# Performance work log

Hardware: AMD Instinct MI355X
Metric: run time of the kernel (lower is better)

The kernel has to match this reference:

```python
import jax, jax.numpy as jnp
import numpy as np

EMB = 1024
HEADS = 16
HEAD_DIM = EMB // HEADS
SEQ = 2048
BATCH = 2
FF = 4 * EMB


def gelu_tanh(x):
    # matches the hand-rolled GELU: 0.5*x*(1+tanh(sqrt(2/pi)*(x+0.044715*x^3)))
    c = jnp.sqrt(jnp.asarray(2.0 / jnp.pi, dtype=x.dtype))
    return 0.5 * x * (1.0 + jnp.tanh(c * (x + 0.044715 * x ** 3)))


def layernorm(x, scale, shift, eps=1e-5):
    mean = jnp.mean(x, axis=-1, keepdims=True)
    var = jnp.var(x, axis=-1, keepdims=True)  # unbiased=False
    return scale * (x - mean) * jax.lax.rsqrt(var + eps) + shift


def setup_inputs() -> dict:
    key = jax.random.key(0)
    ks = jax.random.split(key, 10)
    s = 1.0 / np.sqrt(EMB)
    sf = 1.0 / np.sqrt(FF)
    return {
        "x": jax.random.normal(ks[0], (BATCH, SEQ, EMB), jnp.float32),
        "Wq": jax.random.uniform(ks[1], (EMB, EMB), jnp.float32, -s, s),
        "Wk": jax.random.uniform(ks[2], (EMB, EMB), jnp.float32, -s, s),
        "Wv": jax.random.uniform(ks[3], (EMB, EMB), jnp.float32, -s, s),
        "Wo": jax.random.uniform(ks[4], (EMB, EMB), jnp.float32, -s, s),
        "bo": jnp.zeros((EMB,), jnp.float32),
        "ln1_g": jnp.ones((EMB,), jnp.float32),
        "ln1_b": jnp.zeros((EMB,), jnp.float32),
        "ln2_g": jnp.ones((EMB,), jnp.float32),
        "ln2_b": jnp.zeros((EMB,), jnp.float32),
        "W1": jax.random.uniform(ks[5], (EMB, FF), jnp.float32, -s, s),
        "b1": jnp.zeros((FF,), jnp.float32),
        "W2": jax.random.uniform(ks[6], (FF, EMB), jnp.float32, -sf, sf),
        "b2": jnp.zeros((EMB,), jnp.float32),
    }


def reference(x, Wq, Wk, Wv, Wo, bo, ln1_g, ln1_b, ln2_g, ln2_b, W1, b1, W2, b2):
    b, n, d = x.shape
    shortcut = x
    h = layernorm(x, ln1_g, ln1_b)
    # projections -> [b, heads, n, head_dim]
    def split_heads(t):
        return t.reshape(b, n, HEADS, HEAD_DIM).transpose(0, 2, 1, 3)
    q = split_heads(h @ Wq)
    k = split_heads(h @ Wk)
    v = split_heads(h @ Wv)
    scores = jnp.einsum("bhqd,bhkd->bhqk", q, k)
    causal = jnp.triu(jnp.ones((n, n), dtype=bool), k=1)
    scores = jnp.where(causal, -jnp.inf, scores)
    weights = jax.nn.softmax(scores / jnp.sqrt(jnp.asarray(HEAD_DIM, x.dtype)), axis=-1)
    ctx = jnp.einsum("bhqk,bhkd->bhqd", weights, v)
    ctx = ctx.transpose(0, 2, 1, 3).reshape(b, n, d)
    attn_out = ctx @ Wo + bo
    x = attn_out + shortcut
    shortcut = x
    h = layernorm(x, ln2_g, ln2_b)
    ff = gelu_tanh(h @ W1 + b1) @ W2 + b2
    return ff + shortcut
```

## Files before the change

kernel.cpp:

```cpp
#include <hip/hip_runtime.h>

typedef __bf16 bf16x8 __attribute__((ext_vector_type(8)));
typedef float f32x4 __attribute__((ext_vector_type(4)));
typedef float f32x16 __attribute__((ext_vector_type(16)));
typedef unsigned int u32x4 __attribute__((ext_vector_type(4)));
typedef unsigned short u16;

#define EMB 1024
#define SEQ 2048
#define BATCH 2
#define HEADS 16
#define HEAD_DIM 64
#define FF 4096
#define ROWS (BATCH * SEQ)

#define QSCALE 0.18033688011112042f

static __device__ __forceinline__ u16 f2bf(float f) {
    unsigned int u = __builtin_bit_cast(unsigned int, f);
    unsigned int r = (u + 0x7FFFu + ((u >> 16) & 1u)) >> 16;
    return (u16)r;
}

static __device__ __forceinline__ unsigned int pack_bf_trunc(float a, float b) {
    return __builtin_amdgcn_perm(__builtin_bit_cast(unsigned int, a),
                                 __builtin_bit_cast(unsigned int, b), 0x07060302u);
}

static __device__ __forceinline__ void gload16(const u16* g, u16* l) {
    __builtin_amdgcn_global_load_lds(
        (const __attribute__((address_space(1))) unsigned int*)(const void*)g,
        (__attribute__((address_space(3))) unsigned int*)(void*)l, 16, 0, 0);
}

__global__ __launch_bounds__(256) void transpose_f32_to_bf16(
    const float* __restrict__ in, u16* __restrict__ out, int R, int C) {
    __shared__ float tile[32][33];
    int c0 = blockIdx.x * 32, r0 = blockIdx.y * 32;
    int tx = threadIdx.x & 31, ty = threadIdx.x >> 5;
#pragma unroll
    for (int i = 0; i < 32; i += 8)
        tile[ty + i][tx] = in[(size_t)(r0 + ty + i) * C + c0 + tx];
    __syncthreads();
#pragma unroll
    for (int i = 0; i < 32; i += 8)
        out[(size_t)(c0 + ty + i) * R + r0 + tx] = f2bf(tile[tx][ty + i]);
}

__global__ __launch_bounds__(256) void transpose4_f32_to_bf16(
    const float* __restrict__ s0, const float* __restrict__ s1,
    const float* __restrict__ s2, const float* __restrict__ s3,
    u16* __restrict__ d0, u16* __restrict__ d1,
    u16* __restrict__ d2, u16* __restrict__ d3) {
    __shared__ float tile[32][33];
    const float* in;
    u16* out;
    switch (blockIdx.z) {
        case 0: in = s0; out = d0; break;
        case 1: in = s1; out = d1; break;
        case 2: in = s2; out = d2; break;
        default: in = s3; out = d3; break;
    }
    int c0 = blockIdx.x * 32, r0 = blockIdx.y * 32;
    int tx = threadIdx.x & 31, ty = threadIdx.x >> 5;
#pragma unroll
    for (int i = 0; i < 32; i += 8)
        tile[ty + i][tx] = in[(size_t)(r0 + ty + i) * EMB + c0 + tx];
    __syncthreads();
#pragma unroll
    for (int i = 0; i < 32; i += 8)
        out[(size_t)(c0 + ty + i) * EMB + r0 + tx] = f2bf(tile[tx][ty + i]);
}

__global__ __launch_bounds__(256) void ln_kernel(
    const float* __restrict__ x, const float* __restrict__ gamma,
    const float* __restrict__ beta, u16* __restrict__ out) {
    int row = blockIdx.x;
    int t = threadIdx.x;
    float4 v = reinterpret_cast<const float4*>(x + (size_t)row * EMB)[t];
    float s = v.x + v.y + v.z + v.w;
    float s2 = v.x * v.x + v.y * v.y + v.z * v.z + v.w * v.w;
#pragma unroll
    for (int off = 1; off < 64; off <<= 1) {
        s += __shfl_xor(s, off);
        s2 += __shfl_xor(s2, off);
    }
    __shared__ float sm[8];
    int wid = t >> 6;
    if ((t & 63) == 0) { sm[wid] = s; sm[wid + 4] = s2; }
    __syncthreads();
    s = sm[0] + sm[1] + sm[2] + sm[3];
    s2 = sm[4] + sm[5] + sm[6] + sm[7];
    float mean = s * (1.0f / EMB);
    float var = s2 * (1.0f / EMB) - mean * mean;
    float inv = rsqrtf(var + 1e-5f);
    float4 gv = reinterpret_cast<const float4*>(gamma)[t];
    float4 bv = reinterpret_cast<const float4*>(beta)[t];
    ushort4 o;
    o.x = f2bf((v.x - mean) * inv * gv.x + bv.x);
    o.y = f2bf((v.y - mean) * inv * gv.y + bv.y);
    o.z = f2bf((v.z - mean) * inv * gv.z + bv.z);
    o.w = f2bf((v.w - mean) * inv * gv.w + bv.w);
    reinterpret_cast<ushort4*>(out + (size_t)row * EMB)[t] = o;
}

template <int EPI, int BN>
__global__ __launch_bounds__(256) void gemm_bf16(
    const u16* __restrict__ A, const u16* __restrict__ B, void* __restrict__ Cout,
    const float* __restrict__ bias, const float* __restrict__ resid,
    void* __restrict__ Cout2, void* __restrict__ Cout3,
    int M, int N, int K) {
    __shared__ u16 As[128 * 64];
    __shared__ u16 Bs[BN * 64];
    constexpr int MI = (BN == 128) ? 4 : 2;
    constexpr int BSW = BN / 32;
    int tm = blockIdx.x * 128;
    int tn = blockIdx.y * BN;
    int t = threadIdx.x;
    int lane = t & 63, wid = t >> 6;
    int wr, wc;
    if constexpr (BN == 128) { wr = (wid >> 1) * 64; wc = (wid & 1) * 64; }
    else { wr = wid * 32; wc = 0; }
    int l15 = lane & 15, g = lane >> 4;
    const u16* Abase = A + (size_t)tm * K;
    const u16* Bbase = B + (size_t)tn * K;
    f32x4 acc[MI][4] = {};
    for (int k0 = 0; k0 < K; k0 += 64) {
        __syncthreads();
#pragma unroll
        for (int p = 0; p < 4; ++p) {
            int chunk = (wid * 4 + p) * 64 + lane;
            int row = chunk >> 3, c8 = (chunk & 7) * 8;
            gload16(Abase + (size_t)row * K + k0 + c8, &As[(wid * 4 + p) * 512]);
        }
#pragma unroll
        for (int p = 0; p < BSW; ++p) {
            int chunk = (wid * BSW + p) * 64 + lane;
            int row = chunk >> 3, c8 = (chunk & 7) * 8;
            gload16(Bbase + (size_t)row * K + k0 + c8, &Bs[(wid * BSW + p) * 512]);
        }
        __syncthreads();
#pragma unroll
        for (int kc = 0; kc < 2; ++kc) {
            int ko = kc * 32 + g * 8;
            bf16x8 af[MI], bfr[4];
#pragma unroll
            for (int i = 0; i < MI; ++i)
                af[i] = *reinterpret_cast<const bf16x8*>(&As[(wr + i * 16 + l15) * 64 + ko]);
#pragma unroll
            for (int j = 0; j < 4; ++j)
                bfr[j] = *reinterpret_cast<const bf16x8*>(&Bs[(wc + j * 16 + l15) * 64 + ko]);
#pragma unroll
            for (int i = 0; i < MI; ++i)
#pragma unroll
                for (int j = 0; j < 4; ++j)
                    acc[i][j] = __builtin_amdgcn_mfma_f32_16x16x32_bf16(af[i], bfr[j], acc[i][j], 0, 0, 0);
        }
    }
    int mb = tm + wr + g * 4;
    int nb = tn + wc + l15;
#pragma unroll
    for (int i = 0; i < MI; ++i) {
#pragma unroll
        for (int j = 0; j < 4; ++j) {
            int n = nb + j * 16;
#pragma unroll
            for (int r = 0; r < 4; ++r) {
                int m = mb + i * 16 + r;
                float val = acc[i][j][r];
                if constexpr (EPI == 0) {
                    ((u16*)Cout)[(size_t)m * N + n] = f2bf(val);
                } else if constexpr (EPI == 1) {
                    ((float*)Cout)[(size_t)m * N + n] =
                        val + bias[n] + resid[(size_t)m * N + n];
                } else if constexpr (EPI == 2) {
                    float xg = val + bias[n];
                    float x3 = xg + 0.044715f * xg * xg * xg;
                    float tz = 0.7978845608028654f * x3;
                    float th = 1.0f - 2.0f / (1.0f + __expf(2.0f * tz));
                    ((u16*)Cout)[(size_t)m * N + n] = f2bf(0.5f * xg * (1.0f + th));
                } else {
                    if (n < 1024) {
                        ((u16*)Cout)[(size_t)m * 1024 + n] = f2bf(val * QSCALE);
                    } else if (n < 2048) {
                        ((u16*)Cout2)[(size_t)m * 1024 + (n - 1024)] = f2bf(val);
                    } else {
                        int bb = m >> 11, ss = m & 2047;
                        ((u16*)Cout3)[((size_t)(bb * EMB + (n - 2048))) * SEQ + ss] = f2bf(val);
                    }
                }
            }
        }
    }
}

__global__ __launch_bounds__(64, 2) void attn_kernel(
    const u16* __restrict__ Qb, const u16* __restrict__ Kb,
    const u16* __restrict__ Vt, u16* __restrict__ ctx) {
    int bh = blockIdx.x;
    int b = bh >> 4, h = bh & 15;
    int qc = 63 - (int)blockIdx.y;
    int lane = threadIdx.x;
    int l31 = lane & 31, hi = lane >> 5;
    int hi8 = hi * 8, hi4 = hi * 4;
    int qbase = qc * 32;

    const u16* Qrow = Qb + (size_t)(b * SEQ) * EMB + h * 64;
    const u16* Krow = Kb + (size_t)(b * SEQ) * EMB + h * 64;
    const u16* Vrow = Vt + (size_t)(b * EMB + h * 64) * SEQ;

    bf16x8 qf[4];
#pragma unroll
    for (int kc = 0; kc < 4; ++kc)
        qf[kc] = *reinterpret_cast<const bf16x8*>(
            Qrow + (size_t)(qbase + l31) * EMB + kc * 16 + hi8);

    f32x16 ctx_acc[2] = {};
    float mrun = -1e30f;
    float lrun = 0.f;
    int nkt = qc / 2 + 1;

    bf16x8 kcur[8];
#pragma unroll
    for (int i = 0; i < 8; ++i) {
        int kb = i >> 2, kc = i & 3;
        kcur[i] = *reinterpret_cast<const bf16x8*>(
            Krow + (size_t)(kb * 32 + l31) * EMB + kc * 16 + hi8);
    }

    for (int kt = 0; kt < nkt; ++kt) {
        int k0 = kt * 64;
        bool last = (kt == nkt - 1);
        bf16x8 vf[8];
#pragma unroll
        for (int i = 0; i < 8; ++i) {
            int ks = i >> 1, dt = i & 1;
            vf[i] = *reinterpret_cast<const bf16x8*>(
                Vrow + (size_t)(dt * 32 + l31) * SEQ + k0 + ks * 16 + hi8);
        }
        f32x16 sacc[2] = {};
#pragma unroll
        for (int kb = 0; kb < 2; ++kb)
#pragma unroll
            for (int kc = 0; kc < 4; ++kc)
                sacc[kb] = __builtin_amdgcn_mfma_f32_32x32x16_bf16(
                    kcur[kb * 4 + kc], qf[kc], sacc[kb], 0, 0, 0);
        if (kt + 1 < nkt) {
#pragma unroll
            for (int i = 0; i < 8; ++i) {
                int kb = i >> 2, kc = i & 3;
                kcur[i] = *reinterpret_cast<const bf16x8*>(
                    Krow + (size_t)(k0 + 64 + kb * 32 + l31) * EMB + kc * 16 + hi8);
            }
        }
        float sv[32];
        float tmax = -1e30f;
        if (last) {
            int q = qbase + l31;
#pragma unroll
            for (int kb = 0; kb < 2; ++kb)
#pragma unroll
                for (int r = 0; r < 16; ++r) {
                    int key = k0 + kb * 32 + (r & 3) + 8 * (r >> 2) + hi4;
                    float sx = (key > q) ? -1e30f : sacc[kb][r];
                    sv[kb * 16 + r] = sx;
                    tmax = fmaxf(tmax, sx);
                }
        } else {
#pragma unroll
            for (int kb = 0; kb < 2; ++kb)
#pragma unroll
                for (int r = 0; r < 16; ++r) {
                    float sx = sacc[kb][r];
                    sv[kb * 16 + r] = sx;
                    tmax = fmaxf(tmax, sx);
                }
        }
        tmax = fmaxf(tmax, __shfl_xor(tmax, 32));
        if (!__all(tmax <= mrun + 8.0f)) {
            float mnew = fmaxf(mrun, tmax);
            float corr = __builtin_amdgcn_exp2f(mrun - mnew);
            mrun = mnew;
            lrun *= corr;
            float corr_r[16];
#pragma unroll
            for (int r = 0; r < 16; ++r)
                corr_r[r] = __shfl(corr, (r & 3) + 8 * (r >> 2) + hi4);
#pragma unroll
            for (int dt = 0; dt < 2; ++dt)
#pragma unroll
                for (int r = 0; r < 16; ++r) ctx_acc[dt][r] *= corr_r[r];
        }
        float m = mrun;
        float psum = 0.f;
#pragma unroll
        for (int i = 0; i < 32; ++i) {
            float p = __builtin_amdgcn_exp2f(sv[i] - m);
            sv[i] = p;
            psum += p;
        }
        lrun += psum;
        bf16x8 pa[4];
#pragma unroll
        for (int ks = 0; ks < 4; ++ks) {
            int bse = (ks >> 1) * 16 + (ks & 1) * 8;
            unsigned int w0 = pack_bf_trunc(sv[bse + 1], sv[bse + 0]);
            unsigned int wA = pack_bf_trunc(sv[bse + 5], sv[bse + 4]);
            unsigned int w1 = pack_bf_trunc(sv[bse + 3], sv[bse + 2]);
            unsigned int wB = pack_bf_trunc(sv[bse + 7], sv[bse + 6]);
            asm("v_permlane32_swap_b32 %0, %1" : "+v"(w0), "+v"(wA));
            asm("v_permlane32_swap_b32 %0, %1" : "+v"(w1), "+v"(wB));
            u32x4 words = {w0, w1, wA, wB};
            pa[ks] = __builtin_bit_cast(bf16x8, words);
        }
#pragma unroll
        for (int ks = 0; ks < 4; ++ks)
#pragma unroll
            for (int dt = 0; dt < 2; ++dt)
                ctx_acc[dt] = __builtin_amdgcn_mfma_f32_32x32x16_bf16(
                    pa[ks], vf[ks * 2 + dt], ctx_acc[dt], 0, 0, 0);
    }
    lrun += __shfl_xor(lrun, 32);
    float linv = 1.0f / lrun;
    float li[16];
#pragma unroll
    for (int r = 0; r < 16; ++r)
        li[r] = __shfl(linv, (r & 3) + 8 * (r >> 2) + hi4);
#pragma unroll
    for (int dt = 0; dt < 2; ++dt)
#pragma unroll
        for (int r = 0; r < 16; ++r) {
            int q = qbase + (r & 3) + 8 * (r >> 2) + hi4;
            int d = h * 64 + dt * 32 + l31;
            ctx[(size_t)(b * SEQ + q) * EMB + d] = f2bf(ctx_acc[dt][r] * li[r]);
        }
}

extern "C" void kernel_launch(void* const* d_in, const int* in_sizes, int n_in,
                              void* d_out, int out_size, void* d_ws, size_t ws_size,
                              hipStream_t stream) {
    const float* x    = (const float*)d_in[0];
    const float* Wq   = (const float*)d_in[1];
    const float* Wk   = (const float*)d_in[2];
    const float* Wv   = (const float*)d_in[3];
    const float* Wo   = (const float*)d_in[4];
    const float* bo   = (const float*)d_in[5];
    const float* ln1g = (const float*)d_in[6];
    const float* ln1b = (const float*)d_in[7];
    const float* ln2g = (const float*)d_in[8];
    const float* ln2b = (const float*)d_in[9];
    const float* W1   = (const float*)d_in[10];
    const float* b1   = (const float*)d_in[11];
    const float* W2   = (const float*)d_in[12];
    const float* b2   = (const float*)d_in[13];

    char* ws = (char*)d_ws;
    size_t off = 0;
    auto alloc = [&](size_t bytes) {
        void* p = ws + off;
        off += (bytes + 255) & ~(size_t)255;
        return p;
    };
    u16* h1     = (u16*)alloc((size_t)ROWS * EMB * 2);
    u16* Wqkvt  = (u16*)alloc((size_t)3 * EMB * EMB * 2);
    u16* Wot    = (u16*)alloc((size_t)EMB * EMB * 2);
    u16* W1t    = (u16*)alloc((size_t)FF * EMB * 2);
    u16* W2t    = (u16*)alloc((size_t)EMB * FF * 2);
    u16* Qb     = (u16*)alloc((size_t)ROWS * EMB * 2);
    u16* Kb     = (u16*)alloc((size_t)ROWS * EMB * 2);
    u16* Vtb    = (u16*)alloc((size_t)BATCH * EMB * SEQ * 2);
    u16* ctxb   = (u16*)alloc((size_t)ROWS * EMB * 2);
    float* x2   = (float*)alloc((size_t)ROWS * EMB * 4);
    u16* h2     = (u16*)alloc((size_t)ROWS * EMB * 2);
    u16* ff1    = (u16*)alloc((size_t)ROWS * FF * 2);

    u16* Wqt = Wqkvt;
    u16* Wkt = Wqkvt + (size_t)EMB * EMB;
    u16* Wvt = Wqkvt + (size_t)2 * EMB * EMB;

    transpose4_f32_to_bf16<<<dim3(32, 32, 4), 256, 0, stream>>>(
        Wq, Wk, Wv, Wo, Wqt, Wkt, Wvt, Wot);
    transpose_f32_to_bf16<<<dim3(128, 32), 256, 0, stream>>>(W1, W1t, EMB, FF);
    transpose_f32_to_bf16<<<dim3(32, 128), 256, 0, stream>>>(W2, W2t, FF, EMB);

    ln_kernel<<<ROWS, 256, 0, stream>>>(x, ln1g, ln1b, h1);

    gemm_bf16<4, 128><<<dim3(32, 24), 256, 0, stream>>>(h1, Wqkvt, Qb, nullptr, nullptr,
                                                        Kb, Vtb, ROWS, 3072, EMB);

    attn_kernel<<<dim3(32, 64), 64, 0, stream>>>(Qb, Kb, Vtb, ctxb);

    gemm_bf16<1, 64><<<dim3(32, 16), 256, 0, stream>>>(ctxb, Wot, x2, bo, x,
                                                       nullptr, nullptr, ROWS, EMB, EMB);

    ln_kernel<<<ROWS, 256, 0, stream>>>(x2, ln2g, ln2b, h2);

    gemm_bf16<2, 128><<<dim3(32, 32), 256, 0, stream>>>(h2, W1t, ff1, b1, nullptr,
                                                        nullptr, nullptr, ROWS, FF, EMB);
    gemm_bf16<1, 64><<<dim3(32, 16), 256, 0, stream>>>(ff1, W2t, (float*)d_out, b2, x2,
                                                       nullptr, nullptr, ROWS, EMB, FF);
}
```

Before: 412.9 us.

## Use 64x64 GEMM tiles for N=1024 projections and 32-key attention tiles

Adds a BM template parameter so the Wo and W2 projection GEMMs run with 64x64 tiles, doubling the block count to fill more compute units. The attention kernel now iterates over 32-key tiles instead of 64, cutting wasted work on the causal diagonal tile and lowering register use. In exchange, the smaller GEMM tiles reduce operand reuse, and attention runs more loop iterations with more per-iteration softmax overhead.

New measurement: 414.9 us. About the same (+0.5%).

```diff
diff --git a/kernel.cpp b/kernel.cpp
--- a/kernel.cpp
+++ b/kernel.cpp
@@ -104,34 +104,37 @@
     reinterpret_cast<ushort4*>(out + (size_t)row * EMB)[t] = o;
 }
 
-template <int EPI, int BN>
+template <int EPI, int BM, int BN>
 __global__ __launch_bounds__(256) void gemm_bf16(
     const u16* __restrict__ A, const u16* __restrict__ B, void* __restrict__ Cout,
     const float* __restrict__ bias, const float* __restrict__ resid,
     void* __restrict__ Cout2, void* __restrict__ Cout3,
     int M, int N, int K) {
-    __shared__ u16 As[128 * 64];
+    __shared__ u16 As[BM * 64];
     __shared__ u16 Bs[BN * 64];
-    constexpr int MI = (BN == 128) ? 4 : 2;
+    constexpr int MI = (BM == 128 && BN == 128) ? 4 : 2;
+    constexpr int NJ = (BN == 128) ? 4 : ((BM == 128) ? 4 : 2);
+    constexpr int ASW = BM / 32;
     constexpr int BSW = BN / 32;
-    int tm = blockIdx.x * 128;
+    int tm = blockIdx.x * BM;
     int tn = blockIdx.y * BN;
     int t = threadIdx.x;
     int lane = t & 63, wid = t >> 6;
     int wr, wc;
-    if constexpr (BN == 128) { wr = (wid >> 1) * 64; wc = (wid & 1) * 64; }
-    else { wr = wid * 32; wc = 0; }
+    if constexpr (BM == 128 && BN == 128) { wr = (wid >> 1) * 64; wc = (wid & 1) * 64; }
+    else if constexpr (BM == 128) { wr = wid * 32; wc = 0; }
+    else { wr = (wid >> 1) * 32; wc = (wid & 1) * 32; }
     int l15 = lane & 15, g = lane >> 4;
     const u16* Abase = A + (size_t)tm * K;
     const u16* Bbase = B + (size_t)tn * K;
-    f32x4 acc[MI][4] = {};
+    f32x4 acc[MI][NJ] = {};
     for (int k0 = 0; k0 < K; k0 += 64) {
         __syncthreads();
 #pragma unroll
-        for (int p = 0; p < 4; ++p) {
-            int chunk = (wid * 4 + p) * 64 + lane;
+        for (int p = 0; p < ASW; ++p) {
+            int chunk = (wid * ASW + p) * 64 + lane;
             int row = chunk >> 3, c8 = (chunk & 7) * 8;
-            gload16(Abase + (size_t)row * K + k0 + c8, &As[(wid * 4 + p) * 512]);
+            gload16(Abase + (size_t)row * K + k0 + c8, &As[(wid * ASW + p) * 512]);
         }
 #pragma unroll
         for (int p = 0; p < BSW; ++p) {
@@ -143,17 +146,17 @@
 #pragma unroll
         for (int kc = 0; kc < 2; ++kc) {
             int ko = kc * 32 + g * 8;
-            bf16x8 af[MI], bfr[4];
+            bf16x8 af[MI], bfr[NJ];
 #pragma unroll
             for (int i = 0; i < MI; ++i)
                 af[i] = *reinterpret_cast<const bf16x8*>(&As[(wr + i * 16 + l15) * 64 + ko]);
 #pragma unroll
-            for (int j = 0; j < 4; ++j)
+            for (int j = 0; j < NJ; ++j)
                 bfr[j] = *reinterpret_cast<const bf16x8*>(&Bs[(wc + j * 16 + l15) * 64 + ko]);
 #pragma unroll
             for (int i = 0; i < MI; ++i)
 #pragma unroll
-                for (int j = 0; j < 4; ++j)
+                for (int j = 0; j < NJ; ++j)
                     acc[i][j] = __builtin_amdgcn_mfma_f32_16x16x32_bf16(af[i], bfr[j], acc[i][j], 0, 0, 0);
         }
     }
@@ -162,7 +165,7 @@
 #pragma unroll
     for (int i = 0; i < MI; ++i) {
 #pragma unroll
-        for (int j = 0; j < 4; ++j) {
+        for (int j = 0; j < NJ; ++j) {
             int n = nb + j * 16;
 #pragma unroll
             for (int r = 0; r < 4; ++r) {
@@ -218,63 +221,52 @@
     f32x16 ctx_acc[2] = {};
     float mrun = -1e30f;
     float lrun = 0.f;
-    int nkt = qc / 2 + 1;
-
-    bf16x8 kcur[8];
-#pragma unroll
-    for (int i = 0; i < 8; ++i) {
-        int kb = i >> 2, kc = i & 3;
-        kcur[i] = *reinterpret_cast<const bf16x8*>(
-            Krow + (size_t)(kb * 32 + l31) * EMB + kc * 16 + hi8);
-    }
+    int nkt = qc + 1;
+
+    bf16x8 kcur[4];
+#pragma unroll
+    for (int kc = 0; kc < 4; ++kc)
+        kcur[kc] = *reinterpret_cast<const bf16x8*>(
+            Krow + (size_t)l31 * EMB + kc * 16 + hi8);
 
     for (int kt = 0; kt < nkt; ++kt) {
-        int k0 = kt * 64;
+        int k0 = kt * 32;
         bool last = (kt == nkt - 1);
-        bf16x8 vf[8];
-#pragma unroll
-        for (int i = 0; i < 8; ++i) {
+        bf16x8 vf[4];
+#pragma unroll
+        for (int i = 0; i < 4; ++i) {
             int ks = i >> 1, dt = i & 1;
             vf[i] = *reinterpret_cast<const bf16x8*>(
                 Vrow + (size_t)(dt * 32 + l31) * SEQ + k0 + ks * 16 + hi8);
         }
-        f32x16 sacc[2] = {};
-#pragma unroll
-        for (int kb = 0; kb < 2; ++kb)
+        f32x16 sacc = {};
+#pragma unroll
+        for (int kc = 0; kc < 4; ++kc)
+            sacc = __builtin_amdgcn_mfma_f32_32x32x16_bf16(kcur[kc], qf[kc], sacc, 0, 0, 0);
+        if (kt + 1 < nkt) {
 #pragma unroll
             for (int kc = 0; kc < 4; ++kc)
-                sacc[kb] = __builtin_amdgcn_mfma_f32_32x32x16_bf16(
-                    kcur[kb * 4 + kc], qf[kc], sacc[kb], 0, 0, 0);
-        if (kt + 1 < nkt) {
-#pragma unroll
-            for (int i = 0; i < 8; ++i) {
-                int kb = i >> 2, kc = i & 3;
-                kcur[i] = *reinterpret_cast<const bf16x8*>(
-                    Krow + (size_t)(k0 + 64 + kb * 32 + l31) * EMB + kc * 16 + hi8);
-            }
-        }
-        float sv[32];
+                kcur[kc] = *reinterpret_cast<const bf16x8*>(
+                    Krow + (size_t)(k0 + 32 + l31) * EMB + kc * 16 + hi8);
+        }
+        float sv[16];
         float tmax = -1e30f;
         if (last) {
             int q = qbase + l31;
 #pragma unroll
-            for (int kb = 0; kb < 2; ++kb)
-#pragma unroll
-                for (int r = 0; r < 16; ++r) {
-                    int key = k0 + kb * 32 + (r & 3) + 8 * (r >> 2) + hi4;
-                    float sx = (key > q) ? -1e30f : sacc[kb][r];
-                    sv[kb * 16 + r] = sx;
-                    tmax = fmaxf(tmax, sx);
-                }
+            for (int r = 0; r < 16; ++r) {
+                int key = k0 + (r & 3) + 8 * (r >> 2) + hi4;
+                float sx = (key > q) ? -1e30f : sacc[r];
+                sv[r] = sx;
+                tmax = fmaxf(tmax, sx);
+            }
         } else {
 #pragma unroll
-            for (int kb = 0; kb < 2; ++kb)
-#pragma unroll
-                for (int r = 0; r < 16; ++r) {
-                    float sx = sacc[kb][r];
-                    sv[kb * 16 + r] = sx;
-                    tmax = fmaxf(tmax, sx);
-                }
+            for (int r = 0; r < 16; ++r) {
+                float sx = sacc[r];
+                sv[r] = sx;
+                tmax = fmaxf(tmax, sx);
+            }
         }
         tmax = fmaxf(tmax, __shfl_xor(tmax, 32));
         if (!__all(tmax <= mrun + 8.0f)) {
@@ -294,16 +286,16 @@
         float m = mrun;
         float psum = 0.f;
 #pragma unroll
-        for (int i = 0; i < 32; ++i) {
+        for (int i = 0; i < 16; ++i) {
             float p = __builtin_amdgcn_exp2f(sv[i] - m);
             sv[i] = p;
             psum += p;
         }
         lrun += psum;
-        bf16x8 pa[4];
-#pragma unroll
-        for (int ks = 0; ks < 4; ++ks) {
-            int bse = (ks >> 1) * 16 + (ks & 1) * 8;
+        bf16x8 pa[2];
+#pragma unroll
+        for (int ks = 0; ks < 2; ++ks) {
+            int bse = ks * 8;
             unsigned int w0 = pack_bf_trunc(sv[bse + 1], sv[bse + 0]);
             unsigned int wA = pack_bf_trunc(sv[bse + 5], sv[bse + 4]);
             unsigned int w1 = pack_bf_trunc(sv[bse + 3], sv[bse + 2]);
@@ -314,7 +306,7 @@
             pa[ks] = __builtin_bit_cast(bf16x8, words);
         }
 #pragma unroll
-        for (int ks = 0; ks < 4; ++ks)
+        for (int ks = 0; ks < 2; ++ks)
 #pragma unroll
             for (int dt = 0; dt < 2; ++dt)
                 ctx_acc[dt] = __builtin_amdgcn_mfma_f32_32x32x16_bf16(
@@ -385,18 +377,18 @@
 
     ln_kernel<<<ROWS, 256, 0, stream>>>(x, ln1g, ln1b, h1);
 
-    gemm_bf16<4, 128><<<dim3(32, 24), 256, 0, stream>>>(h1, Wqkvt, Qb, nullptr, nullptr,
-                                                        Kb, Vtb, ROWS, 3072, EMB);
+    gemm_bf16<4, 128, 128><<<dim3(32, 24), 256, 0, stream>>>(h1, Wqkvt, Qb, nullptr, nullptr,
+                                                             Kb, Vtb, ROWS, 3072, EMB);
 
     attn_kernel<<<dim3(32, 64), 64, 0, stream>>>(Qb, Kb, Vtb, ctxb);
 
-    gemm_bf16<1, 64><<<dim3(32, 16), 256, 0, stream>>>(ctxb, Wot, x2, bo, x,
-                                                       nullptr, nullptr, ROWS, EMB, EMB);
+    gemm_bf16<1, 64, 64><<<dim3(64, 16), 256, 0, stream>>>(ctxb, Wot, x2, bo, x,
+                                                           nullptr, nullptr, ROWS, EMB, EMB);
 
     ln_kernel<<<ROWS, 256, 0, stream>>>(x2, ln2g, ln2b, h2);
 
-    gemm_bf16<2, 128><<<dim3(32, 32), 256, 0, stream>>>(h2, W1t, ff1, b1, nullptr,
-                                                        nullptr, nullptr, ROWS, FF, EMB);
-    gemm_bf16<1, 64><<<dim3(32, 16), 256, 0, stream>>>(ff1, W2t, (float*)d_out, b2, x2,
-                                                       nullptr, nullptr, ROWS, EMB, FF);
-}
+    gemm_bf16<2, 128, 128><<<dim3(32, 32), 256, 0, stream>>>(h2, W1t, ff1, b1, nullptr,
+                                                             nullptr, nullptr, ROWS, FF, EMB);
+    gemm_bf16<1, 64, 64><<<dim3(64, 16), 256, 0, stream>>>(ff1, W2t, (float*)d_out, b2, x2,
+                                                           nullptr, nullptr, ROWS, EMB, FF);
+}
```
